# Optimization experiments

Measured on AMD Instinct MI355X. Metric: run time of the kernel, lower is better.

Reference implementation:

```python
import jax, jax.numpy as jnp
import numpy as np

B, S, D, H, NL, FE = 2, 1024, 1024, 16, 6, 4
HD = D // H
DFF = D * FE
EPS = 1e-5


def setup_inputs() -> dict:
    key = jax.random.key(0)
    ks = jax.random.split(key, 12)
    sd = 0.02
    n = lambda k, sh: (jax.random.normal(k, sh, jnp.float32) * sd)
    return {
        "x": jax.random.normal(ks[0], (B, S, D), jnp.float32),
        "pos": n(ks[1], (1, S, D)),
        "Wq": n(ks[2], (NL, HD, HD)), "bq": jnp.zeros((NL, HD), jnp.float32),
        "Wk": n(ks[3], (NL, HD, HD)), "bk": jnp.zeros((NL, HD), jnp.float32),
        "Wv": n(ks[4], (NL, HD, HD)), "bv": jnp.zeros((NL, HD), jnp.float32),
        "Wfc": n(ks[5], (NL, D, D)), "bfc": jnp.zeros((NL, D), jnp.float32),
        "ln1_w": jnp.ones((NL, D), jnp.float32), "ln1_b": jnp.zeros((NL, D), jnp.float32),
        "ln2_w": jnp.ones((NL, D), jnp.float32), "ln2_b": jnp.zeros((NL, D), jnp.float32),
        "W1": n(ks[6], (NL, D, DFF)), "b1": jnp.zeros((NL, DFF), jnp.float32),
        "W2": n(ks[7], (NL, DFF, D)), "b2": jnp.zeros((NL, D), jnp.float32),
        "lnf_w": jnp.ones((D,), jnp.float32), "lnf_b": jnp.zeros((D,), jnp.float32),
    }


def _ln(z, w, b):
    m = jnp.mean(z, axis=-1, keepdims=True)
    v = jnp.mean(jnp.square(z - m), axis=-1, keepdims=True)
    return (z - m) * jax.lax.rsqrt(v + EPS) * w + b


def reference(x, pos, Wq, bq, Wk, bk, Wv, bv, Wfc, bfc,
              ln1_w, ln1_b, ln2_w, ln2_b, W1, b1, W2, b2, lnf_w, lnf_b):
    Bx, Sx, Dx = x.shape
    causal = jnp.tril(jnp.ones((Sx, Sx), bool))  # [S,S], broadcast over b,h
    y = x + pos[:, :Sx, :]
    scale = 1.0 / jnp.sqrt(jnp.float32(HD))
    for i in range(NL):
        yh = y.reshape(Bx, Sx, H, HD)
        # per-head Linear with weights SHARED across heads (as in source)
        q = yh @ Wq[i] + bq[i]
        k = yh @ Wk[i] + bk[i]
        v = yh @ Wv[i] + bv[i]
        score = jnp.einsum("bqhd,bkhd->bhqk", q, k)
        # masked_fill(-1e20) BEFORE scaling, as in source
        score = jnp.where(causal, score, jnp.float32(-1e20)) * scale
        attn = jax.nn.softmax(score, axis=-1)
        o = jnp.einsum("bhqk,bkhd->bqhd", attn, v).reshape(Bx, Sx, D)
        o = o @ Wfc[i] + bfc[i]
        add = _ln(o + y, ln1_w[i], ln1_b[i])
        ff = jax.nn.gelu(add @ W1[i] + b1[i], approximate=False) @ W2[i] + b2[i]
        y = _ln(ff + add, ln2_w[i], ln2_b[i])
    return _ln(y, lnf_w, lnf_b)
```

## Files before the change

kernel.cpp:

```cpp
#include <hip/hip_runtime.h>
#include <hip/hip_bf16.h>
#include <math.h>

#define B_   2
#define S_   1024
#define D_   1024
#define H_   16
#define HD_  64
#define NL_  6
#define DFF_ 4096

typedef __bf16 bf16_t;
typedef bf16_t bf16x8 __attribute__((ext_vector_type(8)));
typedef bf16_t bf16x4 __attribute__((ext_vector_type(4)));
typedef float  f32x4  __attribute__((ext_vector_type(4)));

__device__ __forceinline__ float gelu_exact(float x) {
    return 0.5f * x * (1.0f + erff(x * 0.70710678118654752f));
}

__global__ __launch_bounds__(256) void add_pos_kernel(
    const float* __restrict__ x, const float* __restrict__ pos,
    float* __restrict__ y, bf16_t* __restrict__ yb)
{
    int idx = blockIdx.x * 256 + threadIdx.x;
    f32x4 xv = *(const f32x4*)&x[idx * 4];
    f32x4 pv = *(const f32x4*)&pos[(idx & 262143) * 4];
    f32x4 o = xv + pv;
    *(f32x4*)&y[idx * 4] = o;
    *(bf16x4*)&yb[idx * 4] = __builtin_convertvector(o, bf16x4);
}

__global__ __launch_bounds__(256) void qkv_mfma_kernel(
    const bf16_t* __restrict__ yb,
    const float* __restrict__ Wq, const float* __restrict__ bq,
    const float* __restrict__ Wk, const float* __restrict__ bk,
    const float* __restrict__ Wv, const float* __restrict__ bv,
    bf16_t* __restrict__ q, bf16_t* __restrict__ k, bf16_t* __restrict__ v)
{
    __shared__ bf16_t As[128][72];
    __shared__ bf16_t Wt[3][64][72];

    int tid = threadIdx.x;
    long m0 = (long)blockIdx.x * 128;

#pragma unroll
    for (int it = 0; it < 4; ++it) {
        int c = it * 256 + tid;
        int row = c >> 3, col = (c & 7) * 8;
        *(bf16x8*)&As[row][col] = *(const bf16x8*)&yb[(m0 + row) * 64 + col];
    }
#pragma unroll
    for (int it = 0; it < 16; ++it) {
        int i = it * 256 + tid;
        int r = i >> 6, c = i & 63;
        Wt[0][c][r] = (bf16_t)Wq[i];
        Wt[1][c][r] = (bf16_t)Wk[i];
        Wt[2][c][r] = (bf16_t)Wv[i];
    }
    __syncthreads();

    int wave = tid >> 6, lane = tid & 63;
    int quad = lane >> 4, l16 = lane & 15;
    int wm = wave * 32;

    bf16x8 a[2][2];
#pragma unroll
    for (int i = 0; i < 2; ++i)
#pragma unroll
        for (int ks = 0; ks < 2; ++ks)
            a[i][ks] = *(bf16x8*)&As[wm + i * 16 + l16][ks * 32 + quad * 8];

    f32x4 acc[3][2][4];
#pragma unroll
    for (int o = 0; o < 3; ++o)
#pragma unroll
        for (int i = 0; i < 2; ++i)
#pragma unroll
            for (int j = 0; j < 4; ++j) acc[o][i][j] = (f32x4)0.f;

#pragma unroll
    for (int o = 0; o < 3; ++o)
#pragma unroll
        for (int j = 0; j < 4; ++j) {
            bf16x8 b0 = *(bf16x8*)&Wt[o][j * 16 + l16][quad * 8];
            bf16x8 b1 = *(bf16x8*)&Wt[o][j * 16 + l16][32 + quad * 8];
#pragma unroll
            for (int i = 0; i < 2; ++i) {
                acc[o][i][j] = __builtin_amdgcn_mfma_f32_16x16x32_bf16(a[i][0], b0, acc[o][i][j], 0, 0, 0);
                acc[o][i][j] = __builtin_amdgcn_mfma_f32_16x16x32_bf16(a[i][1], b1, acc[o][i][j], 0, 0, 0);
            }
        }

    bf16_t* outs[3] = { q, k, v };
    const float* biases[3] = { bq, bk, bv };
#pragma unroll
    for (int o = 0; o < 3; ++o)
#pragma unroll
        for (int j = 0; j < 4; ++j) {
            int col = j * 16 + l16;
            float bias = biases[o][col];
#pragma unroll
            for (int i = 0; i < 2; ++i) {
                long rbase = m0 + wm + i * 16 + quad * 4;
#pragma unroll
                for (int r = 0; r < 4; ++r)
                    outs[o][(rbase + r) * 64 + col] = (bf16_t)(acc[o][i][j][r] + bias);
            }
        }
}

__global__ __launch_bounds__(256) void attn_mfma_kernel(
    const bf16_t* __restrict__ Q, const bf16_t* __restrict__ K,
    const bf16_t* __restrict__ V, bf16_t* __restrict__ Ob)
{
    __shared__ bf16_t Ks[32][72];
    __shared__ bf16_t Vt[64][40];
    __shared__ bf16_t Ps[4][16][40];

    int tid = threadIdx.x;
    int wave = tid >> 6, lane = tid & 63;
    int quad = lane >> 4, l16 = lane & 15;
    int q0 = blockIdx.x * 64;
    int bh = blockIdx.y;
    int b = bh >> 4, h = bh & 15;
    int qw = q0 + wave * 16;
    const float scale = 0.125f;
    const float MASKED = -1.25e19f;

    const bf16_t* Qbase = Q + (((long)b * S_ + qw + l16) * H_ + h) * HD_;
    bf16x8 aq0 = *(const bf16x8*)&Qbase[quad * 8];
    bf16x8 aq1 = *(const bf16x8*)&Qbase[32 + quad * 8];

    float mrun[4], lrun[4];
    f32x4 oacc[4];
#pragma unroll
    for (int r = 0; r < 4; ++r) { mrun[r] = -3.0e38f; lrun[r] = 0.f; }
#pragma unroll
    for (int n = 0; n < 4; ++n) oacc[n] = (f32x4)0.f;

    int srow = tid >> 3, scol = (tid & 7) * 8;
    int nkt = (q0 + 64) / 32;
    for (int kt = 0; kt < nkt; ++kt) {
        int k0 = kt * 32;
        __syncthreads();
        {
            long base = (((long)b * S_ + k0 + srow) * H_ + h) * HD_ + scol;
            *(bf16x8*)&Ks[srow][scol] = *(const bf16x8*)&K[base];
            bf16x8 vv = *(const bf16x8*)&V[base];
#pragma unroll
            for (int j = 0; j < 8; ++j) Vt[scol + j][srow] = vv[j];
        }
        __syncthreads();

        f32x4 sc[2];
        sc[0] = (f32x4)0.f; sc[1] = (f32x4)0.f;
#pragma unroll
        for (int n = 0; n < 2; ++n) {
            bf16x8 bk0 = *(bf16x8*)&Ks[n * 16 + l16][quad * 8];
            bf16x8 bk1 = *(bf16x8*)&Ks[n * 16 + l16][32 + quad * 8];
            sc[n] = __builtin_amdgcn_mfma_f32_16x16x32_bf16(aq0, bk0, sc[n], 0, 0, 0);
            sc[n] = __builtin_amdgcn_mfma_f32_16x16x32_bf16(aq1, bk1, sc[n], 0, 0, 0);
        }

        float alpha[4];
#pragma unroll
        for (int r = 0; r < 4; ++r) {
            int qg = qw + quad * 4 + r;
            float s0 = (k0 + l16      <= qg) ? sc[0][r] * scale : MASKED;
            float s1 = (k0 + 16 + l16 <= qg) ? sc[1][r] * scale : MASKED;
            float mt = fmaxf(s0, s1);
            mt = fmaxf(mt, __shfl_xor(mt, 1));
            mt = fmaxf(mt, __shfl_xor(mt, 2));
            mt = fmaxf(mt, __shfl_xor(mt, 4));
            mt = fmaxf(mt, __shfl_xor(mt, 8));
            float mnew = fmaxf(mrun[r], mt);
            float p0 = __expf(s0 - mnew);
            float p1 = __expf(s1 - mnew);
            float ls = p0 + p1;
            ls += __shfl_xor(ls, 1);
            ls += __shfl_xor(ls, 2);
            ls += __shfl_xor(ls, 4);
            ls += __shfl_xor(ls, 8);
            alpha[r] = __expf(mrun[r] - mnew);
            lrun[r] = lrun[r] * alpha[r] + ls;
            mrun[r] = mnew;
            int prow = quad * 4 + r;
            Ps[wave][prow][l16]      = (bf16_t)p0;
            Ps[wave][prow][16 + l16] = (bf16_t)p1;
        }
        bf16x8 ap = *(bf16x8*)&Ps[wave][l16][quad * 8];

#pragma unroll
        for (int n = 0; n < 4; ++n) {
            bf16x8 bv = *(bf16x8*)&Vt[n * 16 + l16][quad * 8];
            f32x4 c = oacc[n];
#pragma unroll
            for (int r = 0; r < 4; ++r) c[r] *= alpha[r];
            oacc[n] = __builtin_amdgcn_mfma_f32_16x16x32_bf16(ap, bv, c, 0, 0, 0);
        }
    }

#pragma unroll
    for (int r = 0; r < 4; ++r) {
        float inv = 1.0f / lrun[r];
        long rowbase = (((long)b * S_ + qw + quad * 4 + r) * H_ + h) * HD_;
#pragma unroll
        for (int n = 0; n < 4; ++n)
            Ob[rowbase + n * 16 + l16] = (bf16_t)(oacc[n][r] * inv);
    }
}

__global__ void tconv_kernel(const float* __restrict__ W, bf16_t* __restrict__ Wt,
                             int Kd, int Nd)
{
    __shared__ float t[32][33];
    int tx = threadIdx.x, ty = threadIdx.y;
    int bx = blockIdx.x, by = blockIdx.y;
#pragma unroll
    for (int i = 0; i < 4; ++i)
        t[ty + i * 8][tx] = W[(size_t)(by * 32 + ty + i * 8) * Nd + bx * 32 + tx];
    __syncthreads();
#pragma unroll
    for (int i = 0; i < 4; ++i)
        Wt[(size_t)(bx * 32 + ty + i * 8) * Kd + by * 32 + tx] = (bf16_t)t[tx][ty + i * 8];
}

#define LDT 40
template<int BN>
__global__ __launch_bounds__(256) void gemm_bt_kernel(
    const bf16_t* __restrict__ A, const bf16_t* __restrict__ Bt,
    const float* __restrict__ bias, float* __restrict__ Cf,
    bf16_t* __restrict__ Cb, int M, int N, int K, int act, size_t pstride)
{
    __shared__ bf16_t As[128 * LDT];
    __shared__ bf16_t Bs[BN * LDT];
    int tid = threadIdx.x;
    int wave = tid >> 6, lane = tid & 63;
    int quad = lane >> 4, l16 = lane & 15;
    int m0 = blockIdx.x * 128;
    int n0 = blockIdx.y * BN;
    int Kc = K / gridDim.z;
    int kbeg = blockIdx.z * Kc;
    int kend = kbeg + Kc;
    float* Cfp = Cf ? Cf + (size_t)blockIdx.z * pstride : nullptr;

    constexpr int WN = BN / 2;
    constexpr int NJ = WN / 16;
    int wm = (wave >> 1) * 64, wn = (wave & 1) * WN;

    f32x4 acc[4][NJ];
#pragma unroll
    for (int i = 0; i < 4; ++i)
#pragma unroll
        for (int j = 0; j < NJ; ++j) acc[i][j] = (f32x4)0.f;

    for (int k0 = kbeg; k0 < kend; k0 += 32) {
        __syncthreads();
#pragma unroll
        for (int it = 0; it < 2; ++it) {
            int c = it * 256 + tid;
            int row = c >> 2, col = (c & 3) * 8;
            *(bf16x8*)&As[row * LDT + col] =
                *(const bf16x8*)&A[(size_t)(m0 + row) * K + k0 + col];
        }
#pragma unroll
        for (int it = 0; it < BN / 64; ++it) {
            int c = it * 256 + tid;
            int row = c >> 2, col = (c & 3) * 8;
            *(bf16x8*)&Bs[row * LDT + col] =
                *(const bf16x8*)&Bt[(size_t)(n0 + row) * K + k0 + col];
        }
        __syncthreads();

        bf16x8 af[4], bfr[NJ];
#pragma unroll
        for (int i = 0; i < 4; ++i)
            af[i] = *(bf16x8*)&As[(wm + i * 16 + l16) * LDT + quad * 8];
#pragma unroll
        for (int j = 0; j < NJ; ++j)
            bfr[j] = *(bf16x8*)&Bs[(wn + j * 16 + l16) * LDT + quad * 8];
#pragma unroll
        for (int i = 0; i < 4; ++i)
#pragma unroll
            for (int j = 0; j < NJ; ++j)
                acc[i][j] = __builtin_amdgcn_mfma_f32_16x16x32_bf16(
                    af[i], bfr[j], acc[i][j], 0, 0, 0);
    }

#pragma unroll
    for (int j = 0; j < NJ; ++j) {
        int col = n0 + wn + j * 16 + l16;
        float bv = (bias && blockIdx.z == 0) ? bias[col] : 0.f;
#pragma unroll
        for (int i = 0; i < 4; ++i) {
            int rbase = m0 + wm + i * 16 + quad * 4;
#pragma unroll
            for (int r = 0; r < 4; ++r) {
                float vv = acc[i][j][r] + bv;
                if (act == 1) vv = gelu_exact(vv);
                if (Cfp) Cfp[(size_t)(rbase + r) * N + col] = vv;
                if (Cb) Cb[(size_t)(rbase + r) * N + col] = (bf16_t)vv;
            }
        }
    }
}

__global__ __launch_bounds__(256) void ln_fused_kernel(
    const float* __restrict__ a0, const float* __restrict__ a1,
    const float* __restrict__ b,
    const float* __restrict__ w, const float* __restrict__ beta,
    float* __restrict__ out, bf16_t* __restrict__ outb)
{
    long row = blockIdx.x;
    int tid = threadIdx.x;
    f32x4 z = *(const f32x4*)&a0[row * D_ + tid * 4];
    if (a1) z += *(const f32x4*)&a1[row * D_ + tid * 4];
    if (b)  z += *(const f32x4*)&b[row * D_ + tid * 4];
    float s  = z[0] + z[1] + z[2] + z[3];
    float ss = z[0]*z[0] + z[1]*z[1] + z[2]*z[2] + z[3]*z[3];
#pragma unroll
    for (int off = 32; off >= 1; off >>= 1) {
        s  += __shfl_down(s, off);
        ss += __shfl_down(ss, off);
    }
    __shared__ float red[8];
    int lane = tid & 63, wid = tid >> 6;
    if (lane == 0) { red[wid * 2] = s; red[wid * 2 + 1] = ss; }
    __syncthreads();
    s  = red[0] + red[2] + red[4] + red[6];
    ss = red[1] + red[3] + red[5] + red[7];
    float mean = s * (1.0f / D_);
    float var  = ss * (1.0f / D_) - mean * mean;
    float rs = rsqrtf(var + 1e-5f);
    f32x4 wv = *(const f32x4*)&w[tid * 4];
    f32x4 bv = *(const f32x4*)&beta[tid * 4];
    f32x4 o = (z - mean) * rs * wv + bv;
    *(f32x4*)&out[row * D_ + tid * 4] = o;
    if (outb) *(bf16x4*)&outb[row * D_ + tid * 4] = __builtin_convertvector(o, bf16x4);
}

extern "C" void kernel_launch(void* const* d_in, const int* in_sizes, int n_in,
                              void* d_out, int out_size, void* d_ws, size_t ws_size,
                              hipStream_t stream)
{
    (void)in_sizes; (void)n_in; (void)out_size; (void)ws_size;
    const float* x    = (const float*)d_in[0];
    const float* pos  = (const float*)d_in[1];
    const float* Wq   = (const float*)d_in[2];
    const float* bq   = (const float*)d_in[3];
    const float* Wk   = (const float*)d_in[4];
    const float* bk   = (const float*)d_in[5];
    const float* Wv   = (const float*)d_in[6];
    const float* bv   = (const float*)d_in[7];
    const float* Wfc  = (const float*)d_in[8];
    const float* bfc  = (const float*)d_in[9];
    const float* ln1w = (const float*)d_in[10];
    const float* ln1b = (const float*)d_in[11];
    const float* ln2w = (const float*)d_in[12];
    const float* ln2b = (const float*)d_in[13];
    const float* W1   = (const float*)d_in[14];
    const float* b1   = (const float*)d_in[15];
    const float* W2   = (const float*)d_in[16];
    const float* b2   = (const float*)d_in[17];
    const float* lnfw = (const float*)d_in[18];
    const float* lnfb = (const float*)d_in[19];

    const size_t MB = 1 << 20;
    char* ws = (char*)d_ws;
    float*  y    = (float*)(ws);
    bf16_t* yb   = (bf16_t*)(ws + 8 * MB);
    bf16_t* qb   = (bf16_t*)(ws + 12 * MB);
    bf16_t* kb   = (bf16_t*)(ws + 16 * MB);
    bf16_t* vb   = (bf16_t*)(ws + 20 * MB);
    bf16_t* ob   = (bf16_t*)(ws + 24 * MB);
    float*  t1a  = (float*)(ws + 12 * MB);
    float*  t1b  = (float*)(ws + 28 * MB);
    float*  t2a  = (float*)(ws + 12 * MB);
    float*  t2b  = (float*)(ws + 20 * MB);
    float*  add  = (float*)(ws + 28 * MB);
    bf16_t* addb = (bf16_t*)(ws + 36 * MB);
    bf16_t* ffb  = (bf16_t*)(ws + 40 * MB);
    bf16_t* WT   = (bf16_t*)(ws + 56 * MB);

    const size_t pstride_wfc  = (size_t)16 * MB / sizeof(float);
    const size_t pstride_ffn2 = (size_t)8 * MB / sizeof(float);

    add_pos_kernel<<<2048, 256, 0, stream>>>(x, pos, y, yb);

    for (int i = 0; i < NL_; ++i) {
        qkv_mfma_kernel<<<256, 256, 0, stream>>>(
            yb, Wq + i * 4096, bq + i * 64, Wk + i * 4096, bk + i * 64,
            Wv + i * 4096, bv + i * 64, qb, kb, vb);

        attn_mfma_kernel<<<dim3(16, 32), 256, 0, stream>>>(qb, kb, vb, ob);

        tconv_kernel<<<dim3(32, 32), dim3(32, 8), 0, stream>>>(
            Wfc + (size_t)i * D_ * D_, WT, D_, D_);
        gemm_bt_kernel<64><<<dim3(16, 16, 2), 256, 0, stream>>>(
            ob, WT, bfc + i * D_, t1a, nullptr, 2048, D_, D_, 0, pstride_wfc);

        ln_fused_kernel<<<2048, 256, 0, stream>>>(
            t1a, t1b, y, ln1w + i * D_, ln1b + i * D_, add, addb);

        tconv_kernel<<<dim3(128, 32), dim3(32, 8), 0, stream>>>(
            W1 + (size_t)i * D_ * DFF_, WT, D_, DFF_);
        gemm_bt_kernel<128><<<dim3(16, 32, 1), 256, 0, stream>>>(
            addb, WT, b1 + i * DFF_, nullptr, ffb, 2048, DFF_, D_, 1, 0);

        tconv_kernel<<<dim3(32, 128), dim3(32, 8), 0, stream>>>(
            W2 + (size_t)i * DFF_ * D_, WT, DFF_, D_);
        gemm_bt_kernel<64><<<dim3(16, 16, 2), 256, 0, stream>>>(
            ffb, WT, b2 + i * D_, t2a, nullptr, 2048, D_, DFF_, 0, pstride_ffn2);

        ln_fused_kernel<<<2048, 256, 0, stream>>>(
            t2a, t2b, add, ln2w + i * D_, ln2b + i * D_, y, yb);
    }

    ln_fused_kernel<<<2048, 256, 0, stream>>>(
        y, nullptr, nullptr, lnfw, lnfb, (float*)d_out, nullptr);
}
```

Baseline: 1.480 ms.

## Pre-transpose V and restructure attention softmax to a transposed score layout

Adds a separate kernel that writes V into a per-head transposed [bh][d][s] layout, so the attention kernel loads Vt tiles with vector copies instead of scalar scattered shared-memory writes. The QK^T MFMA operands are swapped so each lane holds one query column, which cuts softmax row reductions from four 16-lane shuffle trees to two cross-quad shuffles and lets probabilities be stored as packed bf16x4. Waves whose 16 query rows lie entirely above a causal-masked key tile now skip the compute. The cost is an extra kernel launch and an extra V read and write per layer; the vT buffer reuses workspace shared with ffb, which is safe only because ffb is written later in the layer.

```diff
diff --git a/kernel.cpp b/kernel.cpp
--- a/kernel.cpp
+++ b/kernel.cpp
@@ -110,9 +110,28 @@
         }
 }
 
+__global__ __launch_bounds__(256) void vtrans_kernel(
+    const bf16_t* __restrict__ vb, bf16_t* __restrict__ vT)
+{
+    __shared__ bf16_t L[32][72];
+    int tid = threadIdx.x;
+    int s0 = blockIdx.x * 32;
+    int bh = blockIdx.y;
+    int b = bh >> 4, h = bh & 15;
+    int sr = tid >> 3, dc = (tid & 7) * 8;
+    *(bf16x8*)&L[sr][dc] =
+        *(const bf16x8*)&vb[(((long)b * S_ + s0 + sr) * H_ + h) * HD_ + dc];
+    __syncthreads();
+    int dr = tid >> 2, sg = (tid & 3) * 8;
+    bf16x8 o;
+#pragma unroll
+    for (int j = 0; j < 8; ++j) o[j] = L[sg + j][dr];
+    *(bf16x8*)&vT[((long)bh * HD_ + dr) * S_ + s0 + sg] = o;
+}
+
 __global__ __launch_bounds__(256) void attn_mfma_kernel(
     const bf16_t* __restrict__ Q, const bf16_t* __restrict__ K,
-    const bf16_t* __restrict__ V, bf16_t* __restrict__ Ob)
+    const bf16_t* __restrict__ VT, bf16_t* __restrict__ Ob)
 {
     __shared__ bf16_t Ks[32][72];
     __shared__ bf16_t Vt[64][40];
@@ -132,82 +151,89 @@
     bf16x8 aq0 = *(const bf16x8*)&Qbase[quad * 8];
     bf16x8 aq1 = *(const bf16x8*)&Qbase[32 + quad * 8];
 
-    float mrun[4], lrun[4];
+    float mrun = -3.0e38f, lrun = 0.f;
     f32x4 oacc[4];
 #pragma unroll
-    for (int r = 0; r < 4; ++r) { mrun[r] = -3.0e38f; lrun[r] = 0.f; }
-#pragma unroll
     for (int n = 0; n < 4; ++n) oacc[n] = (f32x4)0.f;
 
     int srow = tid >> 3, scol = (tid & 7) * 8;
+    int vdr = tid >> 2, vkg = (tid & 3) * 8;
+    const bf16_t* VTbase = VT + ((long)bh * HD_ + vdr) * S_ + vkg;
+    int qg = qw + l16;
+
     int nkt = (q0 + 64) / 32;
     for (int kt = 0; kt < nkt; ++kt) {
         int k0 = kt * 32;
         __syncthreads();
-        {
-            long base = (((long)b * S_ + k0 + srow) * H_ + h) * HD_ + scol;
-            *(bf16x8*)&Ks[srow][scol] = *(const bf16x8*)&K[base];
-            bf16x8 vv = *(const bf16x8*)&V[base];
-#pragma unroll
-            for (int j = 0; j < 8; ++j) Vt[scol + j][srow] = vv[j];
-        }
+        *(bf16x8*)&Ks[srow][scol] =
+            *(const bf16x8*)&K[(((long)b * S_ + k0 + srow) * H_ + h) * HD_ + scol];
+        *(bf16x8*)&Vt[vdr][vkg] = *(const bf16x8*)&VTbase[k0];
         __syncthreads();
+
+        if (k0 > qw + 15) continue;
 
         f32x4 sc[2];
         sc[0] = (f32x4)0.f; sc[1] = (f32x4)0.f;
 #pragma unroll
         for (int n = 0; n < 2; ++n) {
-            bf16x8 bk0 = *(bf16x8*)&Ks[n * 16 + l16][quad * 8];
-            bf16x8 bk1 = *(bf16x8*)&Ks[n * 16 + l16][32 + quad * 8];
-            sc[n] = __builtin_amdgcn_mfma_f32_16x16x32_bf16(aq0, bk0, sc[n], 0, 0, 0);
-            sc[n] = __builtin_amdgcn_mfma_f32_16x16x32_bf16(aq1, bk1, sc[n], 0, 0, 0);
-        }
-
-        float alpha[4];
-#pragma unroll
-        for (int r = 0; r < 4; ++r) {
-            int qg = qw + quad * 4 + r;
-            float s0 = (k0 + l16      <= qg) ? sc[0][r] * scale : MASKED;
-            float s1 = (k0 + 16 + l16 <= qg) ? sc[1][r] * scale : MASKED;
-            float mt = fmaxf(s0, s1);
-            mt = fmaxf(mt, __shfl_xor(mt, 1));
-            mt = fmaxf(mt, __shfl_xor(mt, 2));
-            mt = fmaxf(mt, __shfl_xor(mt, 4));
-            mt = fmaxf(mt, __shfl_xor(mt, 8));
-            float mnew = fmaxf(mrun[r], mt);
-            float p0 = __expf(s0 - mnew);
-            float p1 = __expf(s1 - mnew);
-            float ls = p0 + p1;
-            ls += __shfl_xor(ls, 1);
-            ls += __shfl_xor(ls, 2);
-            ls += __shfl_xor(ls, 4);
-            ls += __shfl_xor(ls, 8);
-            alpha[r] = __expf(mrun[r] - mnew);
-            lrun[r] = lrun[r] * alpha[r] + ls;
-            mrun[r] = mnew;
-            int prow = quad * 4 + r;
-            Ps[wave][prow][l16]      = (bf16_t)p0;
-            Ps[wave][prow][16 + l16] = (bf16_t)p1;
-        }
-        bf16x8 ap = *(bf16x8*)&Ps[wave][l16][quad * 8];
-
+            bf16x8 ak0 = *(bf16x8*)&Ks[n * 16 + l16][quad * 8];
+            bf16x8 ak1 = *(bf16x8*)&Ks[n * 16 + l16][32 + quad * 8];
+            sc[n] = __builtin_amdgcn_mfma_f32_16x16x32_bf16(ak0, aq0, sc[n], 0, 0, 0);
+            sc[n] = __builtin_amdgcn_mfma_f32_16x16x32_bf16(ak1, aq1, sc[n], 0, 0, 0);
+        }
+        float pmax = MASKED;
+#pragma unroll
+        for (int n = 0; n < 2; ++n)
+#pragma unroll
+            for (int r = 0; r < 4; ++r) {
+                int kv = k0 + n * 16 + quad * 4 + r;
+                float sv = (kv <= qg) ? sc[n][r] * scale : MASKED;
+                sc[n][r] = sv;
+                pmax = fmaxf(pmax, sv);
+            }
+        pmax = fmaxf(pmax, __shfl_xor(pmax, 16));
+        pmax = fmaxf(pmax, __shfl_xor(pmax, 32));
+        float mnew = fmaxf(mrun, pmax);
+        float ls = 0.f;
+#pragma unroll
+        for (int n = 0; n < 2; ++n)
+#pragma unroll
+            for (int r = 0; r < 4; ++r) {
+                float pv = __expf(sc[n][r] - mnew);
+                sc[n][r] = pv;
+                ls += pv;
+            }
+        ls += __shfl_xor(ls, 16);
+        ls += __shfl_xor(ls, 32);
+        float alpha = __expf(mrun - mnew);
+        lrun = lrun * alpha + ls;
+        mrun = mnew;
+
+        *(bf16x4*)&Ps[wave][l16][quad * 4]      = __builtin_convertvector(sc[0], bf16x4);
+        *(bf16x4*)&Ps[wave][l16][16 + quad * 4] = __builtin_convertvector(sc[1], bf16x4);
+
+        f32x4 av;
+#pragma unroll
+        for (int r = 0; r < 4; ++r) av[r] = __shfl(alpha, quad * 4 + r);
+
+        bf16x8 pa = *(bf16x8*)&Ps[wave][l16][quad * 8];
 #pragma unroll
         for (int n = 0; n < 4; ++n) {
             bf16x8 bv = *(bf16x8*)&Vt[n * 16 + l16][quad * 8];
-            f32x4 c = oacc[n];
-#pragma unroll
-            for (int r = 0; r < 4; ++r) c[r] *= alpha[r];
-            oacc[n] = __builtin_amdgcn_mfma_f32_16x16x32_bf16(ap, bv, c, 0, 0, 0);
-        }
-    }
-
+            oacc[n] = __builtin_amdgcn_mfma_f32_16x16x32_bf16(pa, bv, oacc[n] * av, 0, 0, 0);
+        }
+    }
+
+    float inv = 1.0f / lrun;
+    f32x4 iv;
+#pragma unroll
+    for (int r = 0; r < 4; ++r) iv[r] = __shfl(inv, quad * 4 + r);
 #pragma unroll
     for (int r = 0; r < 4; ++r) {
-        float inv = 1.0f / lrun[r];
         long rowbase = (((long)b * S_ + qw + quad * 4 + r) * H_ + h) * HD_;
 #pragma unroll
         for (int n = 0; n < 4; ++n)
-            Ob[rowbase + n * 16 + l16] = (bf16_t)(oacc[n][r] * inv);
+            Ob[rowbase + n * 16 + l16] = (bf16_t)(oacc[n][r] * iv[r]);
     }
 }
 
@@ -380,6 +406,7 @@
     float*  t2b  = (float*)(ws + 20 * MB);
     float*  add  = (float*)(ws + 28 * MB);
     bf16_t* addb = (bf16_t*)(ws + 36 * MB);
+    bf16_t* vTb  = (bf16_t*)(ws + 40 * MB);
     bf16_t* ffb  = (bf16_t*)(ws + 40 * MB);
     bf16_t* WT   = (bf16_t*)(ws + 56 * MB);
 
@@ -393,7 +420,9 @@
             yb, Wq + i * 4096, bq + i * 64, Wk + i * 4096, bk + i * 64,
             Wv + i * 4096, bv + i * 64, qb, kb, vb);
 
-        attn_mfma_kernel<<<dim3(16, 32), 256, 0, stream>>>(qb, kb, vb, ob);
+        vtrans_kernel<<<dim3(32, 32), 256, 0, stream>>>(vb, vTb);
+
+        attn_mfma_kernel<<<dim3(16, 32), 256, 0, stream>>>(qb, kb, vTb, ob);
 
         tconv_kernel<<<dim3(32, 32), dim3(32, 8), 0, stream>>>(
             Wfc + (size_t)i * D_ * D_, WT, D_, D_);
```

Measured after the change: 1.354 ms. 1.09x faster.
